# Performance work log

Hardware: AMD Instinct MI355X
Metric: run time of the kernel (lower is better)

## Reference

```python
import jax, jax.numpy as jnp
import numpy as np

DN = ('NCHW', 'OIHW', 'NCHW')
THRESHOLD = 20   # Broyden iterations (hardcoded in the torch forward)


def conv(x, k):
    return jax.lax.conv_general_dilated(x, k, (1, 1), 'SAME', dimension_numbers=DN)


def _matvec(Us, VTs, v):
    # (-I + Us @ VTs) v ; Us [B,D,K], VTs [B,K,D], v [B,D]
    return -v + jnp.einsum('bdk,bk->bd', Us, jnp.einsum('bkd,bd->bk', VTs, v))


def _rmatvec(Us, VTs, v):
    # v^T (-I + Us @ VTs)
    return -v + jnp.einsum('bk,bkd->bd', jnp.einsum('bd,bdk->bk', v, Us), VTs)


def broyden_solve(g, x0, threshold):
    """Broyden's method with low-rank inverse-Jacobian updates (J^{-1} = -I + Us VTs),
    returning the iterate with the lowest residual norm (as in the DEQ broyden solver)."""
    B, D = x0.shape
    x, gx = x0, g(x0)
    Us = jnp.zeros((B, D, threshold), x0.dtype)
    VTs = jnp.zeros((B, threshold, D), x0.dtype)
    best_x, best_obj = x, jnp.linalg.norm(gx)
    update = gx  # -(-I) gx with empty low-rank part
    for k in range(threshold):
        x_new = x + update
        gx_new = g(x_new)
        dx, dgx = x_new - x, gx_new - gx
        vT = _rmatvec(Us, VTs, dx)                       # [B,D]
        denom = jnp.einsum('bd,bd->b', vT, dgx)[:, None]
        denom = jnp.where(jnp.abs(denom) < 1e-9, 1e-9, denom)
        u = (dx - _matvec(Us, VTs, dgx)) / denom
        Us = Us.at[:, :, k].set(u)
        VTs = VTs.at[:, k, :].set(vT)
        x, gx = x_new, gx_new
        obj = jnp.linalg.norm(gx)
        best_x = jnp.where(obj < best_obj, x, best_x)
        best_obj = jnp.minimum(obj, best_obj)
        update = -_matvec(Us, VTs, gx)
    return best_x


def setup_inputs() -> dict:
    key = jax.random.key(0)
    k1, k2, k3, k4 = jax.random.split(key, 4)
    B, Cin, Cout, H, W = 16, 64, 128, 32, 32
    x = jax.random.normal(k1, (B, Cin, H, W), jnp.float32)
    # small-norm A so relu(conv(z,A)+...) is a contraction -> equilibrium exists
    A = jax.random.normal(k2, (Cout, Cout, 3, 3), jnp.float32) * 0.02
    U = jax.random.normal(k3, (Cout, Cin, 3, 3), jnp.float32) * 0.05
    b = jax.random.normal(k4, (1, Cout, 1, 1), jnp.float32) * 0.1
    return {'x': x, 'A': A, 'U': U, 'b': b}


def reference(x, A, U, b):
    B, _, H, W = x.shape
    Cout = A.shape[0]
    D = Cout * H * W
    ux = conv(x, U) + b  # input injection, constant over iterations

    def g(zvec):  # residual g(z) = relu(Wz + Ux + b) - z, flattened
        z = zvec.reshape(B, Cout, H, W)
        return (jax.nn.relu(conv(z, A) + ux) - z).reshape(B, D)

    z0 = jnp.zeros((B, D), x.dtype)
    zstar = broyden_solve(g, z0, THRESHOLD).reshape(B, Cout, H, W)
    # final recompute with the equilibrium (the torch code re-runs linear+nonlin)
    zn = jax.nn.relu(conv(zstar, A) + ux)
    return zn
```

## Files before the change

kernel.cpp:

```cpp
#include <hip/hip_runtime.h>
#include <hip/hip_fp16.h>

#define NB    16
#define CIN_  64
#define COUT_ 128
#define PLANE_ 1024
#define DDIM  (COUT_*PLANE_)
#define BDTOT ((size_t)NB*DDIM)
#define KMAX  20
#define NROWS 19
#define SMAX  16
#define SEG   (DDIM / SMAX)
#define CBLK  128
#define PADC  8

typedef short  bfrag __attribute__((ext_vector_type(8)));
typedef float  ffrag __attribute__((ext_vector_type(4)));

__device__ __forceinline__ float bf2f(unsigned short h) {
    return __uint_as_float(((unsigned int)h) << 16);
}
__device__ __forceinline__ unsigned short f2bf(float f) {
    unsigned int u = __float_as_uint(f);
    u = (u + 0x7FFFu + ((u >> 16) & 1u)) >> 16;
    return (unsigned short)u;
}
__device__ __forceinline__ void bf2x(unsigned int w, float& lo, float& hi) {
    lo = __uint_as_float(w << 16);
    hi = __uint_as_float(w & 0xffff0000u);
}
__device__ __forceinline__ unsigned int packbf(float lo, float hi) {
    return ((unsigned int)f2bf(hi) << 16) | (unsigned int)f2bf(lo);
}
__device__ __forceinline__ void ub4(ushort4 a, float* f) {
    f[0] = bf2f(a.x); f[1] = bf2f(a.y); f[2] = bf2f(a.z); f[3] = bf2f(a.w);
}
__device__ __forceinline__ ushort4 pk4(const float* f) {
    ushort4 r; r.x = f2bf(f[0]); r.y = f2bf(f[1]); r.z = f2bf(f[2]); r.w = f2bf(f[3]);
    return r;
}
__device__ __forceinline__ void ub8(uint4 a, float* f) {
    bf2x(a.x, f[0], f[1]); bf2x(a.y, f[2], f[3]);
    bf2x(a.z, f[4], f[5]); bf2x(a.w, f[6], f[7]);
}
__device__ __forceinline__ float wred(float v) {
    #pragma unroll
    for (int m = 32; m > 0; m >>= 1) v += __shfl_xor(v, m, 64);
    return v;
}

__device__ __forceinline__ unsigned char f2bf8(float v) {
    v = fminf(fmaxf(v, -57344.f), 57344.f);
    unsigned short hb = __half_as_ushort(__float2half_rn(v));
    return (unsigned char)((hb + 0x7Fu + ((hb >> 8) & 1u)) >> 8);
}
__device__ __forceinline__ float bf82f(unsigned char b) {
    return __half2float(__ushort_as_half((unsigned short)((unsigned int)b << 8)));
}
__device__ __forceinline__ void ub8f8(uint2 m, float* f) {
    #pragma unroll
    for (int j = 0; j < 4; ++j) f[j]     = bf82f((unsigned char)(m.x >> (8 * j)));
    #pragma unroll
    for (int j = 0; j < 4; ++j) f[4 + j] = bf82f((unsigned char)(m.y >> (8 * j)));
}
__device__ __forceinline__ uint2 pk8f8(const float* f) {
    unsigned int lo = 0, hi = 0;
    #pragma unroll
    for (int j = 0; j < 4; ++j) {
        lo |= (unsigned int)f2bf8(f[j])     << (8 * j);
        hi |= (unsigned int)f2bf8(f[4 + j]) << (8 * j);
    }
    return make_uint2(lo, hi);
}

template<int CIN>
__device__ __forceinline__ void conv_stage_lds(
    const unsigned short* __restrict__ zsrc, unsigned short* lds,
    int hrow, int n, int tid)
{
    const int CP = CIN + PADC;
    const int CH8 = CIN / 8;
    for (int idx = tid; idx < 102 * CH8; idx += 256) {
        int slot = idx / CH8, chunk = idx - slot * CH8;
        int row = slot / 34, pxm = slot - row * 34;
        int h = hrow + row - 1, w = pxm - 1;
        uint4 val = {0u, 0u, 0u, 0u};
        if ((unsigned)h < 32u && (unsigned)w < 32u)
            val = *(const uint4*)(zsrc + ((size_t)n * PLANE_ + h * 32 + w) * CIN + chunk * 8);
        *(uint4*)(lds + (slot)*CP + chunk * 8) = val;
    }
    __syncthreads();
}

template<int CIN>
__device__ __forceinline__ void conv_compute_lds(
    const unsigned short* lds, const unsigned short* __restrict__ Wt,
    int co_base, int col, int quad, ffrag accs[4])
{
    const int CP = CIN + PADC;
    #pragma unroll
    for (int cb = 0; cb < CIN; cb += 32) {
        #pragma unroll
        for (int tap = 0; tap < 9; ++tap) {
            const int dh = tap / 3, dwi = tap % 3;
            const unsigned short* wr0 =
                Wt + ((size_t)tap * COUT_ + co_base + col) * CIN + quad * 8 + cb;
            bfrag a0 = *(const bfrag*)(wr0);
            bfrag a1 = *(const bfrag*)(wr0 + 16 * CIN);
            bfrag b0 = *(const bfrag*)(lds + (dh * 34 + col + dwi) * CP + cb + quad * 8);
            bfrag b1 = *(const bfrag*)(lds + (dh * 34 + col + 16 + dwi) * CP + cb + quad * 8);
            accs[0] = __builtin_amdgcn_mfma_f32_16x16x32_bf16(a0, b0, accs[0], 0, 0, 0);
            accs[1] = __builtin_amdgcn_mfma_f32_16x16x32_bf16(a0, b1, accs[1], 0, 0, 0);
            accs[2] = __builtin_amdgcn_mfma_f32_16x16x32_bf16(a1, b0, accs[2], 0, 0, 0);
            accs[3] = __builtin_amdgcn_mfma_f32_16x16x32_bf16(a1, b1, accs[3], 0, 0, 0);
        }
    }
}

__global__ __launch_bounds__(256) void conv_ux_kernel(
    const unsigned short* __restrict__ xinb, const unsigned short* __restrict__ WU,
    const float* __restrict__ bias, float* __restrict__ ux,
    unsigned short* __restrict__ uxb)
{
    __shared__ unsigned short lds[3 * 34 * (CIN_ + PADC)];
    const int hrow = blockIdx.x, n = blockIdx.y;
    const int tid = threadIdx.x, lane = tid & 63, wv = tid >> 6;
    const int col = lane & 15, quad = lane >> 4;
    conv_stage_lds<CIN_>(xinb, lds, hrow, n, tid);
    ffrag accs[4] = {{0.f,0.f,0.f,0.f},{0.f,0.f,0.f,0.f},{0.f,0.f,0.f,0.f},{0.f,0.f,0.f,0.f}};
    conv_compute_lds<CIN_>(lds, WU, wv * 32, col, quad, accs);
    #pragma unroll
    for (int f = 0; f < 4; ++f) {
        const int mt = f >> 1, nt = f & 1;
        const int co = wv * 32 + mt * 16 + quad * 4;
        const int px = hrow * 32 + nt * 16 + col;
        const size_t o = ((size_t)n * PLANE_ + px) * COUT_ + co;
        float4 bv = *(const float4*)(bias + co);
        float r[4] = {accs[f][0] + bv.x, accs[f][1] + bv.y, accs[f][2] + bv.z, accs[f][3] + bv.w};
        *(float4*)(ux + o) = make_float4(r[0], r[1], r[2], r[3]);
        *(ushort4*)(uxb + o) = pk4(r);
    }
}

__global__ __launch_bounds__(256) void conv_bro_kernel(
    const unsigned short* __restrict__ zb, const unsigned short* __restrict__ WA,
    const unsigned short* __restrict__ uxb,
    unsigned short* gxb,
    const unsigned short* __restrict__ updb,
    unsigned short* __restrict__ dgxb,
    float* __restrict__ cparts)
{
    __shared__ unsigned short lds[3 * 34 * (COUT_ + PADC)];
    const int CP = COUT_ + PADC;
    const int hrow = blockIdx.x, n = blockIdx.y;
    const int tid = threadIdx.x, lane = tid & 63, wv = tid >> 6;
    const int col = lane & 15, quad = lane >> 4;
    conv_stage_lds<COUT_>(zb, lds, hrow, n, tid);
    ffrag accs[4] = {{0.f,0.f,0.f,0.f},{0.f,0.f,0.f,0.f},{0.f,0.f,0.f,0.f},{0.f,0.f,0.f,0.f}};
    conv_compute_lds<COUT_>(lds, WA, wv * 32, col, quad, accs);

    float s0 = 0.f, s1 = 0.f, s2 = 0.f, s3 = 0.f, s4 = 0.f, s5 = 0.f;
    #pragma unroll
    for (int f = 0; f < 4; ++f) {
        const int mt = f >> 1, nt = f & 1;
        const int co = wv * 32 + mt * 16 + quad * 4;
        const int wpx = nt * 16 + col;
        const int px = hrow * 32 + wpx;
        const size_t o = ((size_t)n * PLANE_ + px) * COUT_ + co;
        float uxv[4], gov[4], udv[4], xcv[4];
        ub4(*(const ushort4*)(uxb + o), uxv);
        ub4(*(const ushort4*)(gxb + o), gov);
        ub4(*(const ushort4*)(updb + o), udv);
        ub4(*(const ushort4*)(lds + (size_t)(35 + wpx) * CP + co), xcv);
        float g[4], dgv[4];
        #pragma unroll
        for (int r = 0; r < 4; ++r) {
            float tv = accs[f][r] + uxv[r];
            tv = tv > 0.f ? tv : 0.f;
            g[r] = tv - xcv[r];
            dgv[r] = g[r] - gov[r];
            s0 += udv[r] * dgv[r];
            s1 += udv[r] * g[r];
            s2 += g[r] * g[r];
            s3 += udv[r] * udv[r];
            s4 += dgv[r] * dgv[r];
            s5 += dgv[r] * g[r];
        }
        *(ushort4*)(gxb + o)  = pk4(g);
        *(ushort4*)(dgxb + o) = pk4(dgv);
    }
    s0 = wred(s0); s1 = wred(s1); s2 = wred(s2);
    s3 = wred(s3); s4 = wred(s4); s5 = wred(s5);
    if (lane == 0) {
        const int blk = hrow * 4 + wv;
        cparts[((size_t)0 * NB + n) * CBLK + blk] = s0;
        cparts[((size_t)1 * NB + n) * CBLK + blk] = s1;
        cparts[((size_t)2 * NB + n) * CBLK + blk] = s2;
        cparts[((size_t)3 * NB + n) * CBLK + blk] = s3;
        cparts[((size_t)4 * NB + n) * CBLK + blk] = s4;
        cparts[((size_t)5 * NB + n) * CBLK + blk] = s5;
    }
}

#define NWA (9 * 128 * 128)
#define NWU (9 * 128 * 64)
#define NXIN (NB * PLANE_ * CIN_)
__global__ __launch_bounds__(256) void prep_kernel(
    const float* __restrict__ A, const float* __restrict__ U,
    const float* __restrict__ x,
    unsigned short* __restrict__ WA, unsigned short* __restrict__ WU,
    unsigned short* __restrict__ xb)
{
    int idx = blockIdx.x * 256 + threadIdx.x;
    if (idx < NWA) {
        int tap = idx / (128 * 128), r = idx % (128 * 128);
        int co = r >> 7, ci = r & 127;
        WA[idx] = f2bf(A[(co * 128 + ci) * 9 + tap]);
    } else if (idx < NWA + NWU) {
        int j = idx - NWA;
        int tap = j / (128 * 64), r = j % (128 * 64);
        int co = r >> 6, ci = r & 63;
        WU[j] = f2bf(U[(co * 64 + ci) * 9 + tap]);
    } else if (idx < NWA + NWU + NXIN) {
        int j = idx - NWA - NWU;
        int n = j >> 16, r = j & 65535;
        int px = r >> 6, ci = r & 63;
        xb[j] = f2bf(x[(n * 64 + ci) * 1024 + px]);
    }
}

__global__ __launch_bounds__(256) void ew_init_kernel(
    const float* __restrict__ ux, unsigned short* __restrict__ gxb,
    unsigned short* __restrict__ updb,
    unsigned short* __restrict__ zb, unsigned short* __restrict__ bestzb,
    float* __restrict__ objinit)
{
    const int tid = threadIdx.x;
    size_t i = ((size_t)blockIdx.x * 256 + tid) * 8;
    float rr[8];
    float ob = 0.f;
    #pragma unroll
    for (int h = 0; h < 2; ++h) {
        float4 u = *(const float4*)(ux + i + h * 4);
        #pragma unroll
        for (int r = 0; r < 4; ++r) {
            float v = (&u.x)[r];
            v = v > 0.f ? v : 0.f;
            v = bf2f(f2bf(v));
            rr[h*4+r] = v;
            ob += v * v;
        }
    }
    uint4 m = {packbf(rr[0],rr[1]), packbf(rr[2],rr[3]), packbf(rr[4],rr[5]), packbf(rr[6],rr[7])};
    *(uint4*)(gxb  + i) = m;
    *(uint4*)(updb + i) = m;
    *(uint4*)(zb   + i) = m;
    uint4 z0 = {0u, 0u, 0u, 0u};
    *(uint4*)(bestzb + i) = z0;

    __shared__ float so[256];
    so[tid] = ob;
    __syncthreads();
    for (int s = 128; s > 0; s >>= 1) {
        if (tid < s) so[tid] += so[tid + s];
        __syncthreads();
    }
    if (tid == 0) objinit[blockIdx.x] = so[0];
}

__global__ __launch_bounds__(256) void dots_kernel(
    const unsigned char* __restrict__ Usf8, const unsigned char* __restrict__ VTsf8,
    const unsigned short* __restrict__ dgxb,
    float* __restrict__ tparts, int k)
{
    const int b = blockIdx.x, y = blockIdx.y, s = blockIdx.z;
    const int tid = threadIdx.x;
    const size_t segbase = (size_t)b * DDIM + (size_t)s * SEG;
    const int row = (y < k) ? y : (y - k);
    const unsigned char* M = ((y < k) ? VTsf8 : Usf8) + (size_t)row * BDTOT + segbase;
    const uint4* m16 = (const uint4*)(M);
    const uint4* d8  = (const uint4*)(dgxb + segbase);
    float s0 = 0.f;
    #pragma unroll
    for (int it = 0; it < SEG / (16 * 256); ++it) {
        int g = it * 256 + tid;
        uint4 mw = m16[g];
        float dv[16];
        ub8(d8[2 * g], dv); ub8(d8[2 * g + 1], dv + 8);
        unsigned int ws[4] = {mw.x, mw.y, mw.z, mw.w};
        #pragma unroll
        for (int c = 0; c < 4; ++c) {
            #pragma unroll
            for (int j = 0; j < 4; ++j) {
                float mv = bf82f((unsigned char)(ws[c] >> (8 * j)));
                s0 = fmaf(mv, dv[c * 4 + j], s0);
            }
        }
    }
    __shared__ float r0[256];
    r0[tid] = s0;
    __syncthreads();
    for (int st = 128; st > 0; st >>= 1) {
        if (tid < st) r0[tid] += r0[tid + st];
        __syncthreads();
    }
    if (tid == 0) tparts[((size_t)y * NB + b) * SMAX + s] = r0[0];
}

__global__ __launch_bounds__(256) void pass2_kernel(
    unsigned char* __restrict__ Usf8, unsigned char* __restrict__ VTsf8,
    unsigned short* updb,
    const unsigned short* __restrict__ dgxb, const unsigned short* __restrict__ gxb,
    unsigned short* __restrict__ zb, unsigned short* __restrict__ bestzb,
    const float* __restrict__ tparts, const float* __restrict__ cparts,
    const float* __restrict__ objinit,
    const float* __restrict__ parr_r, float* __restrict__ parr_w,
    const float* __restrict__ tp_r, float* __restrict__ tp_w,
    const float* __restrict__ hp_r, float* __restrict__ hp_w,
    float* __restrict__ UU, float* __restrict__ obj_arr, int k)
{
    const int b = blockIdx.y;
    const int bx = blockIdx.x;
    const int tid = threadIdx.x;
    const int lane = tid & 63, wv = tid >> 6;

    __shared__ float sq[KMAX], st[KMAX], sp[KMAX], sr[KMAX], sh[KMAX], UUk[KMAX];
    __shared__ float sS[5];
    __shared__ float sden, sc, sflag, sobj, srk;
    __shared__ float red[256];

    {
        float o = 0.f;
        const float* OB = cparts + (size_t)2 * NB * CBLK;
        for (int j = tid; j < NB * CBLK; j += 256) o += OB[j];
        red[tid] = o;
        __syncthreads();
        for (int s = 128; s > 0; s >>= 1) {
            if (tid < s) red[tid] += red[tid + s];
            __syncthreads();
        }
        if (tid == 0) sobj = red[0];
        __syncthreads();
    }
    float obj0 = 0.f;
    if (k == 0) {
        float o = 0.f;
        for (int j = tid; j < 1024; j += 256) o += objinit[j];
        red[tid] = o;
        __syncthreads();
        for (int s = 128; s > 0; s >>= 1) {
            if (tid < s) red[tid] += red[tid + s];
            __syncthreads();
        }
        obj0 = red[0];
        __syncthreads();
    }

    if (tid < k) {
        float qv = 0.f, rv = 0.f;
        #pragma unroll
        for (int s = 0; s < SMAX; ++s) {
            qv += tparts[((size_t)tid * NB + b) * SMAX + s];
            rv += tparts[((size_t)(k + tid) * NB + b) * SMAX + s];
        }
        sq[tid] = qv; sr[tid] = rv;
        st[tid] = qv + tp_r[b * KMAX + tid];
        sh[tid] = rv + hp_r[b * KMAX + tid];
        sp[tid] = parr_r[b * KMAX + tid];
    }
    if (wv == 1) {
        float a0 = 0.f, a1 = 0.f;
        for (int j = lane; j < CBLK; j += 64) {
            a0 += cparts[((size_t)0 * NB + b) * CBLK + j];
            a1 += cparts[((size_t)3 * NB + b) * CBLK + j];
        }
        a0 = wred(a0); a1 = wred(a1);
        if (lane == 0) { sS[0] = a0; sS[2] = a1; }
    } else if (wv == 2) {
        float a0 = 0.f, a1 = 0.f;
        for (int j = lane; j < CBLK; j += 64) {
            a0 += cparts[((size_t)1 * NB + b) * CBLK + j];
            a1 += cparts[((size_t)4 * NB + b) * CBLK + j];
        }
        a0 = wred(a0); a1 = wred(a1);
        if (lane == 0) { sS[1] = a0; sS[3] = a1; }
    } else if (wv == 3) {
        float a0 = 0.f;
        for (int j = lane; j < CBLK; j += 64)
            a0 += cparts[((size_t)5 * NB + b) * CBLK + j];
        a0 = wred(a0);
        if (lane == 0) sS[4] = a0;
    }
    __syncthreads();

    if (tid == 0) {
        float pq = 0.f, pt = 0.f;
        for (int i = 0; i < k; ++i) { pq += sp[i] * sq[i]; pt += sp[i] * st[i]; }
        float den = -sS[0] + pq;
        if (fabsf(den) < 1e-9f) den = 1e-9f;
        sden = den;
        float rk = -sS[1] + pt;
        srk = rk;
        sc = rk / den;
        float best;
        if (k == 0) best = obj0;
        else {
            best = obj_arr[0];
            for (int j = 1; j <= k; ++j) best = fminf(best, obj_arr[j]);
        }
        sflag = (sobj < best) ? 1.f : 0.f;
    }
    __syncthreads();

    const size_t base = (size_t)b * DDIM + ((size_t)bx * 256 + tid) * 8;
    float xd[8], dg[8], gv[8];
    ub8(*(const uint4*)(updb + base), xd);
    ub8(*(const uint4*)(dgxb + base), dg);
    ub8(*(const uint4*)(gxb  + base), gv);

    float S1[8], S2[8], SV[8];
    #pragma unroll
    for (int j = 0; j < 8; ++j) { S1[j] = 0.f; S2[j] = 0.f; SV[j] = 0.f; }

    int i = 0;
    for (; i + 1 < k; i += 2) {
        uint2 mu0 = *(const uint2*)(Usf8  + (size_t)i * BDTOT + base);
        uint2 mv0 = *(const uint2*)(VTsf8 + (size_t)i * BDTOT + base);
        uint2 mu1 = *(const uint2*)(Usf8  + (size_t)(i + 1) * BDTOT + base);
        uint2 mv1 = *(const uint2*)(VTsf8 + (size_t)(i + 1) * BDTOT + base);
        float u0[8], v0[8], u1[8], v1[8];
        ub8f8(mu0, u0); ub8f8(mv0, v0); ub8f8(mu1, u1); ub8f8(mv1, v1);
        float q0 = sq[i], t0 = st[i], p0 = sp[i];
        float q1 = sq[i+1], t1 = st[i+1], p1 = sp[i+1];
        #pragma unroll
        for (int j = 0; j < 8; ++j) {
            S1[j] = fmaf(q0, u0[j], fmaf(q1, u1[j], S1[j]));
            S2[j] = fmaf(t0, u0[j], fmaf(t1, u1[j], S2[j]));
            SV[j] = fmaf(p0, v0[j], fmaf(p1, v1[j], SV[j]));
        }
    }
    if (i < k) {
        float uvals[8], vvals[8];
        ub8f8(*(const uint2*)(Usf8  + (size_t)i * BDTOT + base), uvals);
        ub8f8(*(const uint2*)(VTsf8 + (size_t)i * BDTOT + base), vvals);
        float qi = sq[i], ti = st[i], pi = sp[i];
        #pragma unroll
        for (int j = 0; j < 8; ++j) {
            S1[j] = fmaf(qi, uvals[j], S1[j]);
            S2[j] = fmaf(ti, uvals[j], S2[j]);
            SV[j] = fmaf(pi, vvals[j], SV[j]);
        }
    }

    float vk[8], uk[8], up[8];
    #pragma unroll
    for (int j = 0; j < 8; ++j) {
        vk[j] = -xd[j] + SV[j];
        uk[j] = (xd[j] + dg[j] - S1[j]) / sden;
        up[j] = gv[j] - sc * (xd[j] + dg[j]) - S2[j] + sc * S1[j];
    }
    *(uint2*)(VTsf8 + (size_t)k * BDTOT + base) = pk8f8(vk);
    *(uint2*)(Usf8  + (size_t)k * BDTOT + base) = pk8f8(uk);

    uint4 upw = {packbf(up[0],up[1]), packbf(up[2],up[3]), packbf(up[4],up[5]), packbf(up[6],up[7])};
    *(uint4*)(updb + base) = upw;
    float upr[8];
    ub8(upw, upr);

    uint4 zcur = *(const uint4*)(zb + base);
    float xc[8];
    ub8(zcur, xc);
    if (sflag != 0.f) {
        *(uint4*)(bestzb + base) = zcur;
    }
    float xn[8];
    #pragma unroll
    for (int j = 0; j < 8; ++j) xn[j] = xc[j] + upr[j];
    uint4 zn = {packbf(xn[0],xn[1]), packbf(xn[2],xn[3]), packbf(xn[4],xn[5]), packbf(xn[6],xn[7])};
    *(uint4*)(zb + base) = zn;

    if (bx == 0) {
        const float den = sden, cc = sc;
        if (tid < k) {
            float acc = sp[tid] + sr[tid];
            for (int j = 0; j < k; ++j)
                acc -= sq[j] * UU[((size_t)b * KMAX + j) * KMAX + tid];
            UUk[tid] = acc / den;
        }
        __syncthreads();
        if (tid == 0) {
            float ww = sS[2] + 2.f * sS[0] + sS[3];
            float wg = sS[1] + sS[4];
            float sumqh = 0.f, sumqpr = 0.f, sumqU = 0.f;
            for (int j = 0; j < k; ++j) {
                sumqh += sq[j] * sh[j];
                sumqpr += sq[j] * (sp[j] + sr[j]);
                sumqU += sq[j] * UUk[j];
            }
            float ug = (wg - sumqh) / den;
            float uw = (ww - sumqpr) / den;
            float UUkk = (uw - sumqU) / den;
            for (int l = 0; l < k; ++l) {
                UU[((size_t)b * KMAX + k) * KMAX + l] = UUk[l];
                UU[((size_t)b * KMAX + l) * KMAX + k] = UUk[l];
            }
            UU[((size_t)b * KMAX + k) * KMAX + k] = UUkk;
            float acc = ug - cc * uw;
            for (int l = 0; l < k; ++l)
                acc -= (st[l] - cc * sq[l]) * UUk[l];
            parr_w[b * KMAX + k] = acc;
            tp_w[b * KMAX + k] = srk;
            hp_w[b * KMAX + k] = ug;
            if (b == 0) {
                if (k == 0) obj_arr[0] = obj0;
                obj_arr[k + 1] = sobj;
            }
        }
        if (tid < k) {
            float acc = sh[tid] - cc * (sp[tid] + sr[tid]);
            for (int l = 0; l < k; ++l)
                acc -= (st[l] - cc * sq[l]) * UU[((size_t)b * KMAX + tid) * KMAX + l];
            parr_w[b * KMAX + tid] = acc;
            tp_w[b * KMAX + tid] = st[tid];
            hp_w[b * KMAX + tid] = sh[tid];
        }
    }
}

__global__ __launch_bounds__(256) void final_kernel(
    const float* __restrict__ cparts, const float* __restrict__ obj_arr,
    const unsigned short* __restrict__ zb, const unsigned short* __restrict__ bestzb,
    const unsigned short* __restrict__ WA, const float* __restrict__ ux,
    float* __restrict__ out)
{
    __shared__ unsigned short lds[3 * 34 * (COUT_ + PADC)];
    __shared__ float red[256];
    __shared__ float sflag;
    const int hrow = blockIdx.x, n = blockIdx.y;
    const int tid = threadIdx.x, lane = tid & 63, wv = tid >> 6;
    const int col = lane & 15, quad = lane >> 4;

    float o = 0.f;
    const float* OB = cparts + (size_t)2 * NB * CBLK;
    for (int j = tid; j < NB * CBLK; j += 256) o += OB[j];
    red[tid] = o;
    __syncthreads();
    for (int s = 128; s > 0; s >>= 1) {
        if (tid < s) red[tid] += red[tid + s];
        __syncthreads();
    }
    if (tid == 0) {
        float best = obj_arr[0];
        for (int j = 1; j < KMAX; ++j) best = fminf(best, obj_arr[j]);
        sflag = (red[0] < best) ? 1.f : 0.f;
    }
    __syncthreads();
    const unsigned short* src = (sflag != 0.f) ? zb : bestzb;

    conv_stage_lds<COUT_>(src, lds, hrow, n, tid);
    ffrag accs[4] = {{0.f,0.f,0.f,0.f},{0.f,0.f,0.f,0.f},{0.f,0.f,0.f,0.f},{0.f,0.f,0.f,0.f}};
    conv_compute_lds<COUT_>(lds, WA, wv * 32, col, quad, accs);
    #pragma unroll
    for (int f = 0; f < 4; ++f) {
        const int mt = f >> 1, nt = f & 1;
        const int co = wv * 32 + mt * 16 + quad * 4;
        const int px = hrow * 32 + nt * 16 + col;
        const size_t o2 = ((size_t)n * PLANE_ + px) * COUT_ + co;
        float4 uv = *(const float4*)(ux + o2);
        #pragma unroll
        for (int r = 0; r < 4; ++r) {
            float t = accs[f][r] + (&uv.x)[r];
            out[((size_t)n * COUT_ + co + r) * PLANE_ + px] = t > 0.f ? t : 0.f;
        }
    }
}

extern "C" void kernel_launch(void* const* d_in, const int* in_sizes, int n_in,
                              void* d_out, int out_size, void* d_ws, size_t ws_size,
                              hipStream_t stream)
{
    (void)in_sizes; (void)n_in; (void)out_size; (void)ws_size;
    const float* x  = (const float*)d_in[0];
    const float* A  = (const float*)d_in[1];
    const float* U  = (const float*)d_in[2];
    const float* bb = (const float*)d_in[3];
    float* out = (float*)d_out;

    char* w = (char*)d_ws;
    size_t off = 0;
    auto alloc = [&](size_t bytes) -> void* {
        void* pp = (void*)(w + off);
        off += (bytes + 255) & ~(size_t)255;
        return pp;
    };
    const size_t BDB  = BDTOT * sizeof(float);
    const size_t BDH  = BDTOT * 2;
    float* ux    = (float*)alloc(BDB);
    unsigned short* uxb    = (unsigned short*)alloc(BDH);
    unsigned short* gxb    = (unsigned short*)alloc(BDH);
    unsigned short* updb   = (unsigned short*)alloc(BDH);
    unsigned short* dgxb   = (unsigned short*)alloc(BDH);
    unsigned short* zb     = (unsigned short*)alloc(BDH);
    unsigned short* bestzb = (unsigned short*)alloc(BDH);
    unsigned short* xinb   = (unsigned short*)alloc((size_t)NXIN * 2);
    unsigned short* WA     = (unsigned short*)alloc((size_t)NWA * 2);
    unsigned short* WU     = (unsigned short*)alloc((size_t)NWU * 2);
    unsigned char* Usf8  = (unsigned char*)alloc((size_t)NROWS * BDTOT);
    unsigned char* VTsf8 = (unsigned char*)alloc((size_t)NROWS * BDTOT);
    float* cparts = (float*)alloc((size_t)6 * NB * CBLK * sizeof(float));
    float* tparts = (float*)alloc((size_t)2 * KMAX * NB * SMAX * sizeof(float));
    float* objinit= (float*)alloc(1024 * sizeof(float));
    float* parr0 = (float*)alloc(NB * KMAX * sizeof(float));
    float* parr1 = (float*)alloc(NB * KMAX * sizeof(float));
    float* tp0   = (float*)alloc(NB * KMAX * sizeof(float));
    float* tp1   = (float*)alloc(NB * KMAX * sizeof(float));
    float* hp0   = (float*)alloc(NB * KMAX * sizeof(float));
    float* hp1   = (float*)alloc(NB * KMAX * sizeof(float));
    float* UU    = (float*)alloc((size_t)NB * KMAX * KMAX * sizeof(float));
    float* obj_arr = (float*)alloc((KMAX + 1) * sizeof(float));

    const dim3 CG(32, NB);
    const int I8WG = (int)(BDTOT / (256 * 8));

    prep_kernel<<<(NWA + NWU + NXIN + 255) / 256, 256, 0, stream>>>(A, U, x, WA, WU, xinb);
    conv_ux_kernel<<<CG, 256, 0, stream>>>(xinb, WU, bb, ux, uxb);
    ew_init_kernel<<<I8WG, 256, 0, stream>>>(ux, gxb, updb, zb, bestzb, objinit);

    float* parr[2] = {parr0, parr1};
    float* tp[2]   = {tp0, tp1};
    float* hp[2]   = {hp0, hp1};
    for (int k = 0; k < KMAX; ++k) {
        conv_bro_kernel<<<CG, 256, 0, stream>>>(zb, WA, uxb, gxb, updb, dgxb, cparts);
        if (k < KMAX - 1) {
            if (k > 0)
                dots_kernel<<<dim3(NB, 2 * k, SMAX), 256, 0, stream>>>(
                    Usf8, VTsf8, dgxb, tparts, k);
            pass2_kernel<<<dim3(DDIM / 2048, NB), 256, 0, stream>>>(
                Usf8, VTsf8, updb, dgxb, gxb, zb, bestzb,
                tparts, cparts, objinit,
                parr[k & 1], parr[(k + 1) & 1],
                tp[k & 1], tp[(k + 1) & 1],
                hp[k & 1], hp[(k + 1) & 1],
                UU, obj_arr, k);
        }
    }

    final_kernel<<<CG, 256, 0, stream>>>(cparts, obj_arr, zb, bestzb, WA, ux, out);
}
```

Baseline: 1.120 ms.

## Split conv tiles into half-rows, fuse init into input conv, drop fp32 ux

The per-iteration conv kernel now handles half a row (16 pixels) per block, so the grid doubles to 1024 blocks and there is more parallelism across CUs. The per-block partial-sum count (CBLK) doubles to match. The element-wise init kernel is folded into the input-injection conv epilogue, and the fp32 ux buffer is removed; the final kernel reads the bf16 copy instead. The trade-offs are more weight reads and halo overhead per output, and lower precision of ux in the final output.

```diff
diff --git a/kernel.cpp b/kernel.cpp
--- a/kernel.cpp
+++ b/kernel.cpp
@@ -11,8 +11,9 @@
 #define NROWS 19
 #define SMAX  16
 #define SEG   (DDIM / SMAX)
-#define CBLK  128
+#define CBLK  256
 #define PADC  8
+#define NOBJ  2048
 
 typedef short  bfrag __attribute__((ext_vector_type(8)));
 typedef float  ffrag __attribute__((ext_vector_type(4)));
@@ -119,8 +120,11 @@
 
 __global__ __launch_bounds__(256) void conv_ux_kernel(
     const unsigned short* __restrict__ xinb, const unsigned short* __restrict__ WU,
-    const float* __restrict__ bias, float* __restrict__ ux,
-    unsigned short* __restrict__ uxb)
+    const float* __restrict__ bias,
+    unsigned short* __restrict__ uxb,
+    unsigned short* __restrict__ gxb, unsigned short* __restrict__ updb,
+    unsigned short* __restrict__ zb, unsigned short* __restrict__ bestzb,
+    float* __restrict__ objinit)
 {
     __shared__ unsigned short lds[3 * 34 * (CIN_ + PADC)];
     const int hrow = blockIdx.x, n = blockIdx.y;
@@ -129,6 +133,7 @@
     conv_stage_lds<CIN_>(xinb, lds, hrow, n, tid);
     ffrag accs[4] = {{0.f,0.f,0.f,0.f},{0.f,0.f,0.f,0.f},{0.f,0.f,0.f,0.f},{0.f,0.f,0.f,0.f}};
     conv_compute_lds<CIN_>(lds, WU, wv * 32, col, quad, accs);
+    float ob = 0.f;
     #pragma unroll
     for (int f = 0; f < 4; ++f) {
         const int mt = f >> 1, nt = f & 1;
@@ -137,9 +142,24 @@
         const size_t o = ((size_t)n * PLANE_ + px) * COUT_ + co;
         float4 bv = *(const float4*)(bias + co);
         float r[4] = {accs[f][0] + bv.x, accs[f][1] + bv.y, accs[f][2] + bv.z, accs[f][3] + bv.w};
-        *(float4*)(ux + o) = make_float4(r[0], r[1], r[2], r[3]);
         *(ushort4*)(uxb + o) = pk4(r);
-    }
+        float v[4];
+        #pragma unroll
+        for (int j = 0; j < 4; ++j) {
+            float t = r[j] > 0.f ? r[j] : 0.f;
+            t = bf2f(f2bf(t));
+            v[j] = t;
+            ob += t * t;
+        }
+        ushort4 m = pk4(v);
+        *(ushort4*)(gxb  + o) = m;
+        *(ushort4*)(updb + o) = m;
+        *(ushort4*)(zb   + o) = m;
+        ushort4 z0 = {0, 0, 0, 0};
+        *(ushort4*)(bestzb + o) = z0;
+    }
+    ob = wred(ob);
+    if (lane == 0) objinit[((size_t)n * 32 + hrow) * 4 + wv] = ob;
 }
 
 __global__ __launch_bounds__(256) void conv_bro_kernel(
@@ -150,28 +170,52 @@
     unsigned short* __restrict__ dgxb,
     float* __restrict__ cparts)
 {
-    __shared__ unsigned short lds[3 * 34 * (COUT_ + PADC)];
+    __shared__ unsigned short lds[3 * 18 * (COUT_ + PADC)];
     const int CP = COUT_ + PADC;
-    const int hrow = blockIdx.x, n = blockIdx.y;
+    const int bx = blockIdx.x, n = blockIdx.y;
+    const int hrow = bx >> 1, pxhalf = bx & 1;
     const int tid = threadIdx.x, lane = tid & 63, wv = tid >> 6;
     const int col = lane & 15, quad = lane >> 4;
-    conv_stage_lds<COUT_>(zb, lds, hrow, n, tid);
-    ffrag accs[4] = {{0.f,0.f,0.f,0.f},{0.f,0.f,0.f,0.f},{0.f,0.f,0.f,0.f},{0.f,0.f,0.f,0.f}};
-    conv_compute_lds<COUT_>(lds, WA, wv * 32, col, quad, accs);
+
+    for (int idx = tid; idx < 54 * 16; idx += 256) {
+        int slot = idx >> 4, chunk = idx & 15;
+        int row = slot / 18, lw = slot - row * 18;
+        int h = hrow + row - 1, w = pxhalf * 16 + lw - 1;
+        uint4 val = {0u, 0u, 0u, 0u};
+        if ((unsigned)h < 32u && (unsigned)w < 32u)
+            val = *(const uint4*)(zb + ((size_t)n * PLANE_ + h * 32 + w) * COUT_ + chunk * 8);
+        *(uint4*)(lds + slot * CP + chunk * 8) = val;
+    }
+    __syncthreads();
+
+    ffrag accs[2] = {{0.f,0.f,0.f,0.f},{0.f,0.f,0.f,0.f}};
+    const int co_base = wv * 32;
+    #pragma unroll
+    for (int cb = 0; cb < COUT_; cb += 32) {
+        #pragma unroll
+        for (int tap = 0; tap < 9; ++tap) {
+            const int dh = tap / 3, dwi = tap % 3;
+            const unsigned short* wr0 =
+                WA + ((size_t)tap * COUT_ + co_base + col) * COUT_ + quad * 8 + cb;
+            bfrag a0 = *(const bfrag*)(wr0);
+            bfrag a1 = *(const bfrag*)(wr0 + 16 * COUT_);
+            bfrag b0 = *(const bfrag*)(lds + (dh * 18 + col + dwi) * CP + cb + quad * 8);
+            accs[0] = __builtin_amdgcn_mfma_f32_16x16x32_bf16(a0, b0, accs[0], 0, 0, 0);
+            accs[1] = __builtin_amdgcn_mfma_f32_16x16x32_bf16(a1, b0, accs[1], 0, 0, 0);
+        }
+    }
 
     float s0 = 0.f, s1 = 0.f, s2 = 0.f, s3 = 0.f, s4 = 0.f, s5 = 0.f;
-    #pragma unroll
-    for (int f = 0; f < 4; ++f) {
-        const int mt = f >> 1, nt = f & 1;
-        const int co = wv * 32 + mt * 16 + quad * 4;
-        const int wpx = nt * 16 + col;
-        const int px = hrow * 32 + wpx;
+    const int px = hrow * 32 + pxhalf * 16 + col;
+    #pragma unroll
+    for (int f = 0; f < 2; ++f) {
+        const int co = co_base + f * 16 + quad * 4;
         const size_t o = ((size_t)n * PLANE_ + px) * COUT_ + co;
         float uxv[4], gov[4], udv[4], xcv[4];
         ub4(*(const ushort4*)(uxb + o), uxv);
         ub4(*(const ushort4*)(gxb + o), gov);
         ub4(*(const ushort4*)(updb + o), udv);
-        ub4(*(const ushort4*)(lds + (size_t)(35 + wpx) * CP + co), xcv);
+        ub4(*(const ushort4*)(lds + (size_t)(19 + col) * CP + co), xcv);
         float g[4], dgv[4];
         #pragma unroll
         for (int r = 0; r < 4; ++r) {
@@ -192,7 +236,7 @@
     s0 = wred(s0); s1 = wred(s1); s2 = wred(s2);
     s3 = wred(s3); s4 = wred(s4); s5 = wred(s5);
     if (lane == 0) {
-        const int blk = hrow * 4 + wv;
+        const int blk = bx * 4 + wv;
         cparts[((size_t)0 * NB + n) * CBLK + blk] = s0;
         cparts[((size_t)1 * NB + n) * CBLK + blk] = s1;
         cparts[((size_t)2 * NB + n) * CBLK + blk] = s2;
@@ -229,45 +273,6 @@
     }
 }
 
-__global__ __launch_bounds__(256) void ew_init_kernel(
-    const float* __restrict__ ux, unsigned short* __restrict__ gxb,
-    unsigned short* __restrict__ updb,
-    unsigned short* __restrict__ zb, unsigned short* __restrict__ bestzb,
-    float* __restrict__ objinit)
-{
-    const int tid = threadIdx.x;
-    size_t i = ((size_t)blockIdx.x * 256 + tid) * 8;
-    float rr[8];
-    float ob = 0.f;
-    #pragma unroll
-    for (int h = 0; h < 2; ++h) {
-        float4 u = *(const float4*)(ux + i + h * 4);
-        #pragma unroll
-        for (int r = 0; r < 4; ++r) {
-            float v = (&u.x)[r];
-            v = v > 0.f ? v : 0.f;
-            v = bf2f(f2bf(v));
-            rr[h*4+r] = v;
-            ob += v * v;
-        }
-    }
-    uint4 m = {packbf(rr[0],rr[1]), packbf(rr[2],rr[3]), packbf(rr[4],rr[5]), packbf(rr[6],rr[7])};
-    *(uint4*)(gxb  + i) = m;
-    *(uint4*)(updb + i) = m;
-    *(uint4*)(zb   + i) = m;
-    uint4 z0 = {0u, 0u, 0u, 0u};
-    *(uint4*)(bestzb + i) = z0;
-
-    __shared__ float so[256];
-    so[tid] = ob;
-    __syncthreads();
-    for (int s = 128; s > 0; s >>= 1) {
-        if (tid < s) so[tid] += so[tid + s];
-        __syncthreads();
-    }
-    if (tid == 0) objinit[blockIdx.x] = so[0];
-}
-
 __global__ __launch_bounds__(256) void dots_kernel(
     const unsigned char* __restrict__ Usf8, const unsigned char* __restrict__ VTsf8,
     const unsigned short* __restrict__ dgxb,
@@ -345,7 +350,7 @@
     float obj0 = 0.f;
     if (k == 0) {
         float o = 0.f;
-        for (int j = tid; j < 1024; j += 256) o += objinit[j];
+        for (int j = tid; j < NOBJ; j += 256) o += objinit[j];
         red[tid] = o;
         __syncthreads();
         for (int s = 128; s > 0; s >>= 1) {
@@ -530,7 +535,7 @@
 __global__ __launch_bounds__(256) void final_kernel(
     const float* __restrict__ cparts, const float* __restrict__ obj_arr,
     const unsigned short* __restrict__ zb, const unsigned short* __restrict__ bestzb,
-    const unsigned short* __restrict__ WA, const float* __restrict__ ux,
+    const unsigned short* __restrict__ WA, const unsigned short* __restrict__ uxb,
     float* __restrict__ out)
 {
     __shared__ unsigned short lds[3 * 34 * (COUT_ + PADC)];
@@ -566,10 +571,11 @@
         const int co = wv * 32 + mt * 16 + quad * 4;
         const int px = hrow * 32 + nt * 16 + col;
         const size_t o2 = ((size_t)n * PLANE_ + px) * COUT_ + co;
-        float4 uv = *(const float4*)(ux + o2);
+        float uxv[4];
+        ub4(*(const ushort4*)(uxb + o2), uxv);
         #pragma unroll
         for (int r = 0; r < 4; ++r) {
-            float t = accs[f][r] + (&uv.x)[r];
+            float t = accs[f][r] + uxv[r];
             out[((size_t)n * COUT_ + co + r) * PLANE_ + px] = t > 0.f ? t : 0.f;
         }
     }
@@ -593,9 +599,7 @@
         off += (bytes + 255) & ~(size_t)255;
         return pp;
     };
-    const size_t BDB  = BDTOT * sizeof(float);
     const size_t BDH  = BDTOT * 2;
-    float* ux    = (float*)alloc(BDB);
     unsigned short* uxb    = (unsigned short*)alloc(BDH);
     unsigned short* gxb    = (unsigned short*)alloc(BDH);
     unsigned short* updb   = (unsigned short*)alloc(BDH);
@@ -609,7 +613,7 @@
     unsigned char* VTsf8 = (unsigned char*)alloc((size_t)NROWS * BDTOT);
     float* cparts = (float*)alloc((size_t)6 * NB * CBLK * sizeof(float));
     float* tparts = (float*)alloc((size_t)2 * KMAX * NB * SMAX * sizeof(float));
-    float* objinit= (float*)alloc(1024 * sizeof(float));
+    float* objinit= (float*)alloc((size_t)NOBJ * sizeof(float));
     float* parr0 = (float*)alloc(NB * KMAX * sizeof(float));
     float* parr1 = (float*)alloc(NB * KMAX * sizeof(float));
     float* tp0   = (float*)alloc(NB * KMAX * sizeof(float));
@@ -619,18 +623,16 @@
     float* UU    = (float*)alloc((size_t)NB * KMAX * KMAX * sizeof(float));
     float* obj_arr = (float*)alloc((KMAX + 1) * sizeof(float));
 
-    const dim3 CG(32, NB);
-    const int I8WG = (int)(BDTOT / (256 * 8));
-
     prep_kernel<<<(NWA + NWU + NXIN + 255) / 256, 256, 0, stream>>>(A, U, x, WA, WU, xinb);
-    conv_ux_kernel<<<CG, 256, 0, stream>>>(xinb, WU, bb, ux, uxb);
-    ew_init_kernel<<<I8WG, 256, 0, stream>>>(ux, gxb, updb, zb, bestzb, objinit);
+    conv_ux_kernel<<<dim3(32, NB), 256, 0, stream>>>(
+        xinb, WU, bb, uxb, gxb, updb, zb, bestzb, objinit);
 
     float* parr[2] = {parr0, parr1};
     float* tp[2]   = {tp0, tp1};
     float* hp[2]   = {hp0, hp1};
     for (int k = 0; k < KMAX; ++k) {
-        conv_bro_kernel<<<CG, 256, 0, stream>>>(zb, WA, uxb, gxb, updb, dgxb, cparts);
+        conv_bro_kernel<<<dim3(64, NB), 256, 0, stream>>>(
+            zb, WA, uxb, gxb, updb, dgxb, cparts);
         if (k < KMAX - 1) {
             if (k > 0)
                 dots_kernel<<<dim3(NB, 2 * k, SMAX), 256, 0, stream>>>(
@@ -645,5 +647,6 @@
         }
     }
 
-    final_kernel<<<CG, 256, 0, stream>>>(cparts, obj_arr, zb, bestzb, WA, ux, out);
-}
+    final_kernel<<<dim3(32, NB), 256, 0, stream>>>(
+        cparts, obj_arr, zb, bestzb, WA, uxb, out);
+}
```

Result: slower. 1.438 ms (+28.4%).
